# Kernel tuning notes

Hardware: AMD Instinct MI355X
Metric: run time of the kernel (lower is better)

## Reference

```python
import jax, jax.numpy as jnp
import numpy as np

B, S, H = 32, 128, 768
MH, MT = 6, 8            # max holder / target span sizes
M = max(MH, MT)          # max span size -> M conv widths (1..M)
KH, KT = 4, 4            # max n holders / targets per sentence


def _forward(embedding, mask, wh, bh, wt, bt, wi, bi, we, be):
    Bz, Sz, Hz = embedding.shape
    # --- multi-scale span averaging (Conv1d with identity box filters == moving mean) ---
    cs = jnp.concatenate([jnp.zeros((Bz, 1, Hz), embedding.dtype),
                          jnp.cumsum(embedding, axis=1)], axis=1)  # [B,S+1,H]
    reps = [embedding]
    for w in range(2, M + 1):
        mean = (cs[:, w:, :] - cs[:, :-w, :]) / float(w)          # [B,S-w+1,H]
        reps.append(jnp.pad(mean, ((0, 0), (0, w - 1), (0, 0))))  # zero-pad tail like torch.cat
    span = jnp.concatenate(reps, axis=1)                          # [B, M*S, H]; index = S*width_idx + start
    # --- span validity masks (span must fit within sentence length) ---
    lengths = jnp.sum(mask, axis=1)                               # [B]
    pos = jnp.arange(Sz)
    widths = jnp.arange(M)
    base = pos[None, None, :] < (lengths[:, None, None] - widths[None, :, None])  # [B,M,S]
    holder_valid = (base & (widths[None, :, None] < MH)).reshape(Bz, M * Sz)
    target_valid = (base & (widths[None, :, None] < MT)).reshape(Bz, M * Sz)
    # --- span scoring (sigmoid linear), invalid spans forced to -1 ---
    hs = jnp.where(holder_valid, jax.nn.sigmoid(span @ wh + bh), -1.0)  # [B, M*S]
    ts = jnp.where(target_valid, jax.nn.sigmoid(span @ wt + bt), -1.0)
    # --- top-k span selection (== argsort descending, take first K) ---
    vt, it = jax.lax.top_k(ts, KT)
    vh, ih = jax.lax.top_k(hs, KH)
    tval = vt > 0.0                                                # [B,KT]
    hval = vh > 0.0                                                # [B,KH]
    trep = jnp.take_along_axis(span, it[:, :, None], axis=1)      # [B,KT,H]
    hrep = jnp.take_along_axis(span, ih[:, :, None], axis=1)      # [B,KH,H]
    implicit_input = trep * tval[:, :, None].astype(span.dtype)   # zeros where invalid
    pair_valid = (hval[:, :, None] & tval[:, None, :])            # [B,KH,KT]
    pair = jnp.concatenate([jnp.broadcast_to(hrep[:, :, None, :], (Bz, KH, KT, Hz)),
                            jnp.broadcast_to(trep[:, None, :, :], (Bz, KH, KT, Hz))], axis=-1)
    explicit_input = (pair * pair_valid[..., None].astype(span.dtype)).reshape(Bz, KH * KT, 2 * Hz)
    implicit_logits = implicit_input @ wi + bi                    # [B,KT,4]
    explicit_logits = explicit_input @ we + be                    # [B,KH*KT,4]
    return implicit_logits, explicit_logits, hs, ts


def setup_inputs() -> dict:
    key = jax.random.key(0)
    ks = jax.random.split(key, 8)
    embedding = jax.random.normal(ks[0], (B, S, H), jnp.float32)
    mask = jax.random.randint(ks[1], (B, S), 0, 2).astype(jnp.int32)
    wh = jax.random.normal(ks[2], (H,), jnp.float32) * 0.02
    bh = jnp.zeros((), jnp.float32)
    wt = jax.random.normal(ks[3], (H,), jnp.float32) * 0.02
    bt = jnp.zeros((), jnp.float32)
    wi = jax.random.normal(ks[4], (H, 4), jnp.float32) * 0.02
    bi = jnp.zeros((4,), jnp.float32)
    we = jax.random.normal(ks[5], (2 * H, 4), jnp.float32) * 0.02
    be = jnp.zeros((4,), jnp.float32)
    return dict(embedding=embedding, mask=mask, wh=wh, bh=bh, wt=wt, bt=bt,
                wi=wi, bi=bi, we=we, be=be)


def reference(embedding, mask, wh, bh, wt, bt, wi, bi, we, be):
    return _forward(embedding, mask, wh, bh, wt, bt, wi, bi, we, be)
```

## Files before the change

### kernel.cpp

```cpp
#include <hip/hip_runtime.h>

namespace {
constexpr int Bsz = 32;
constexpr int Ssz = 128;
constexpr int Hsz = 768;
constexpr int Msz = 8;
constexpr int MHs = 6;
constexpr int NSPAN = Msz * Ssz;
}

__device__ __forceinline__ bool gtpair(float av, int ai, float bv, int bi) {
    return (av > bv) || (av == bv && ai < bi);
}

struct Top4 { float v[4]; int ix[4]; };

__device__ __forceinline__ void t4_init(Top4& t) {
#pragma unroll
    for (int k = 0; k < 4; ++k) { t.v[k] = -3.f; t.ix[k] = 0x7fffffff; }
}

__device__ __forceinline__ void t4_insert(Top4& t, float cv, int ci) {
    if (!gtpair(cv, ci, t.v[3], t.ix[3])) return;
    if (gtpair(cv, ci, t.v[2], t.ix[2])) {
        t.v[3] = t.v[2]; t.ix[3] = t.ix[2];
        if (gtpair(cv, ci, t.v[1], t.ix[1])) {
            t.v[2] = t.v[1]; t.ix[2] = t.ix[1];
            if (gtpair(cv, ci, t.v[0], t.ix[0])) {
                t.v[1] = t.v[0]; t.ix[1] = t.ix[0];
                t.v[0] = cv; t.ix[0] = ci;
            } else { t.v[1] = cv; t.ix[1] = ci; }
        } else { t.v[2] = cv; t.ix[2] = ci; }
    } else { t.v[3] = cv; t.ix[3] = ci; }
}

__device__ __forceinline__ Top4 t4_merge(const Top4& a, const Top4& b) {
    Top4 r; int pa = 0, pb = 0;
#pragma unroll
    for (int k = 0; k < 4; ++k) {
        float av = a.v[pa]; int ai = a.ix[pa];
        float bv = b.v[pb]; int bi_ = b.ix[pb];
        bool ta = gtpair(av, ai, bv, bi_);
        r.v[k] = ta ? av : bv;
        r.ix[k] = ta ? ai : bi_;
        pa += ta ? 1 : 0; pb += ta ? 0 : 1;
    }
    return r;
}

__device__ __forceinline__ Top4 t4_wave_merge(Top4 t) {
#pragma unroll
    for (int off = 1; off < 64; off <<= 1) {
        Top4 o;
#pragma unroll
        for (int k = 0; k < 4; ++k) {
            o.v[k]  = __shfl_xor(t.v[k], off);
            o.ix[k] = __shfl_xor(t.ix[k], off);
        }
        t = t4_merge(t, o);
    }
    return t;
}

__global__ __launch_bounds__(256) void row_dots_kernel(
    const float* __restrict__ emb, const float* __restrict__ wh,
    const float* __restrict__ wt, float* __restrict__ dh, float* __restrict__ dt)
{
    int row  = blockIdx.x * 4 + (threadIdx.x >> 6);
    int lane = threadIdx.x & 63;
    const float4* r  = (const float4*)(emb + (size_t)row * Hsz);
    const float4* h4 = (const float4*)wh;
    const float4* t4 = (const float4*)wt;
    float ph = 0.f, pt = 0.f;
#pragma unroll
    for (int i = 0; i < 3; ++i) {
        float4 e = r[lane + 64 * i];
        float4 a = h4[lane + 64 * i];
        float4 c = t4[lane + 64 * i];
        ph = fmaf(e.x, a.x, fmaf(e.y, a.y, fmaf(e.z, a.z, fmaf(e.w, a.w, ph))));
        pt = fmaf(e.x, c.x, fmaf(e.y, c.y, fmaf(e.z, c.z, fmaf(e.w, c.w, pt))));
    }
#pragma unroll
    for (int off = 32; off; off >>= 1) {
        ph += __shfl_down(ph, off);
        pt += __shfl_down(pt, off);
    }
    if (lane == 0) { dh[row] = ph; dt[row] = pt; }
}

__global__ __launch_bounds__(256) void per_batch_kernel(
    const float* __restrict__ emb, const int* __restrict__ mask,
    const float* __restrict__ bh_p, const float* __restrict__ bt_p,
    const float* __restrict__ wi, const float* __restrict__ bi,
    const float* __restrict__ we, const float* __restrict__ be,
    const float* __restrict__ dh, const float* __restrict__ dt,
    float* __restrict__ out)
{
    const int b = blockIdx.x;
    const int tid = threadIdx.x;
    const int wavei = tid >> 6, lane = tid & 63;

    __shared__ float dsh[Ssz], dst_[Ssz];
    __shared__ int   len_s;
    __shared__ float swv[2][4][4];
    __shared__ int   swi[2][4][4];
    __shared__ int   sel[8];
    __shared__ int   val[8];
    __shared__ float proj[8][8];

    if (tid < Ssz) {
        dsh[tid]  = dh[b * Ssz + tid];
        dst_[tid] = dt[b * Ssz + tid];
    }
    if (wavei == 0) {
        int m = mask[b * Ssz + lane] + mask[b * Ssz + lane + 64];
#pragma unroll
        for (int off = 32; off; off >>= 1) m += __shfl_down(m, off);
        if (lane == 0) len_s = m;
    }
    __syncthreads();

    const int   len = len_s;
    const float bhv = bh_p[0], btv = bt_p[0];
    float* out_impl = out;
    float* out_expl = out + Bsz * 16;
    float* out_hs   = out_expl + Bsz * 64;
    float* out_ts   = out_hs + Bsz * NSPAN;

    Top4 tt, th;
    t4_init(tt); t4_init(th);
#pragma unroll
    for (int q = 0; q < 4; ++q) {
        int i = tid + 256 * q;
        int widx = i >> 7, st = i & (Ssz - 1), w = widx + 1;
        float h = -1.f, t = -1.f;
        if (st < len - widx) {
            float s_t = 0.f;
            for (int r = 0; r < w; ++r) s_t += dst_[st + r];
            float xt = s_t / (float)w + btv;
            t = 1.f / (1.f + __expf(-xt));
            if (widx < MHs) {
                float s_h = 0.f;
                for (int r = 0; r < w; ++r) s_h += dsh[st + r];
                float xh = s_h / (float)w + bhv;
                h = 1.f / (1.f + __expf(-xh));
            }
        }
        out_hs[b * NSPAN + i] = h;
        out_ts[b * NSPAN + i] = t;
        t4_insert(tt, t, i);
        t4_insert(th, h, i);
    }
    tt = t4_wave_merge(tt);
    th = t4_wave_merge(th);
    if (lane == 0) {
#pragma unroll
        for (int k = 0; k < 4; ++k) {
            swv[0][wavei][k] = tt.v[k]; swi[0][wavei][k] = tt.ix[k];
            swv[1][wavei][k] = th.v[k]; swi[1][wavei][k] = th.ix[k];
        }
    }
    __syncthreads();

    if (tid < 2) {
        Top4 m;
#pragma unroll
        for (int k = 0; k < 4; ++k) { m.v[k] = swv[tid][0][k]; m.ix[k] = swi[tid][0][k]; }
        for (int w2 = 1; w2 < 4; ++w2) {
            Top4 o;
#pragma unroll
            for (int k = 0; k < 4; ++k) { o.v[k] = swv[tid][w2][k]; o.ix[k] = swi[tid][w2][k]; }
            m = t4_merge(m, o);
        }
#pragma unroll
        for (int k = 0; k < 4; ++k) {
            sel[tid * 4 + k] = m.ix[k];
            val[tid * 4 + k] = (m.v[k] > 0.f) ? 1 : 0;
        }
    }
    __syncthreads();

    for (int s2 = 0; s2 < 2; ++s2) {
        int slot = wavei + 4 * s2;
        float acc[8] = {0.f, 0.f, 0.f, 0.f, 0.f, 0.f, 0.f, 0.f};
        if (val[slot]) {
            int idx = sel[slot];
            int w = (idx >> 7) + 1, st = idx & (Ssz - 1);
            const float* base = emb + ((size_t)b * Ssz + st) * Hsz;
#pragma unroll
            for (int ii = 0; ii < Hsz / 64; ++ii) {
                int d = lane + 64 * ii;
                float s = 0.f;
                for (int r = 0; r < w; ++r) s += base[r * Hsz + d];
                float rep = s / (float)w;
                if (s2 == 0) {
                    float4 w4 = ((const float4*)wi)[d];
                    float4 e4 = ((const float4*)we)[Hsz + d];
                    acc[0] = fmaf(rep, w4.x, acc[0]); acc[1] = fmaf(rep, w4.y, acc[1]);
                    acc[2] = fmaf(rep, w4.z, acc[2]); acc[3] = fmaf(rep, w4.w, acc[3]);
                    acc[4] = fmaf(rep, e4.x, acc[4]); acc[5] = fmaf(rep, e4.y, acc[5]);
                    acc[6] = fmaf(rep, e4.z, acc[6]); acc[7] = fmaf(rep, e4.w, acc[7]);
                } else {
                    float4 e4 = ((const float4*)we)[d];
                    acc[0] = fmaf(rep, e4.x, acc[0]); acc[1] = fmaf(rep, e4.y, acc[1]);
                    acc[2] = fmaf(rep, e4.z, acc[2]); acc[3] = fmaf(rep, e4.w, acc[3]);
                }
            }
        }
#pragma unroll
        for (int off = 32; off; off >>= 1)
#pragma unroll
            for (int c = 0; c < 8; ++c) acc[c] += __shfl_down(acc[c], off);
        if (lane == 0)
#pragma unroll
            for (int c = 0; c < 8; ++c) proj[slot][c] = acc[c];
    }
    __syncthreads();

    if (tid < 16) {
        int k = tid >> 2, c = tid & 3;
        out_impl[b * 16 + tid] = bi[c] + (val[k] ? proj[k][c] : 0.f);
    } else if (tid >= 64 && tid < 128) {
        int u = tid - 64;
        int j = u >> 4, k = (u >> 2) & 3, c = u & 3;
        float v = be[c];
        if (val[4 + j] && val[k]) v += proj[4 + j][c] + proj[k][4 + c];
        out_expl[b * 64 + u] = v;
    }
}

extern "C" void kernel_launch(void* const* d_in, const int* in_sizes, int n_in,
                              void* d_out, int out_size, void* d_ws, size_t ws_size,
                              hipStream_t stream) {
    const float* emb  = (const float*)d_in[0];
    const int*   mask = (const int*)d_in[1];
    const float* wh   = (const float*)d_in[2];
    const float* bh   = (const float*)d_in[3];
    const float* wt   = (const float*)d_in[4];
    const float* bt   = (const float*)d_in[5];
    const float* wi   = (const float*)d_in[6];
    const float* bi   = (const float*)d_in[7];
    const float* we   = (const float*)d_in[8];
    const float* be   = (const float*)d_in[9];
    float* out = (float*)d_out;

    float* dh = (float*)d_ws;
    float* dt = dh + Bsz * Ssz;

    row_dots_kernel<<<(Bsz * Ssz) / 4, 256, 0, stream>>>(emb, wh, wt, dh, dt);
    per_batch_kernel<<<Bsz, 256, 0, stream>>>(emb, mask, bh, bt, wi, bi, we, be,
                                              dh, dt, out);
}
```

Before: 104.2 us.

## Use running prefix sums for span scores and vectorize span gather

Span scoring now assigns each thread a single start position and one score type (target or holder), keeping a running sum across widths. This replaces the per-width inner loops over shared memory. Each wave produces one top-4, and the final merge combines pairs of waves. In the projection stage the span embedding gather uses float4 loads and a fully unrolled width loop that masks rows past the span width, so more loads can be in flight. The cost is redundant loads of the last row for short spans and more registers.

```diff
diff --git a/kernel.cpp b/kernel.cpp
--- a/kernel.cpp
+++ b/kernel.cpp
@@ -102,8 +102,8 @@
 
     __shared__ float dsh[Ssz], dst_[Ssz];
     __shared__ int   len_s;
-    __shared__ float swv[2][4][4];
-    __shared__ int   swi[2][4][4];
+    __shared__ float swv[4][4];
+    __shared__ int   swi[4][4];
     __shared__ int   sel[8];
     __shared__ int   val[8];
     __shared__ float proj[8][8];
@@ -127,51 +127,44 @@
     float* out_hs   = out_expl + Bsz * 64;
     float* out_ts   = out_hs + Bsz * NSPAN;
 
-    Top4 tt, th;
-    t4_init(tt); t4_init(th);
-#pragma unroll
-    for (int q = 0; q < 4; ++q) {
-        int i = tid + 256 * q;
-        int widx = i >> 7, st = i & (Ssz - 1), w = widx + 1;
-        float h = -1.f, t = -1.f;
-        if (st < len - widx) {
-            float s_t = 0.f;
-            for (int r = 0; r < w; ++r) s_t += dst_[st + r];
-            float xt = s_t / (float)w + btv;
-            t = 1.f / (1.f + __expf(-xt));
-            if (widx < MHs) {
-                float s_h = 0.f;
-                for (int r = 0; r < w; ++r) s_h += dsh[st + r];
-                float xh = s_h / (float)w + bhv;
-                h = 1.f / (1.f + __expf(-xh));
+    {
+        const int st  = tid & (Ssz - 1);
+        const int grp = tid >> 7;
+        const float* dar = grp ? dsh : dst_;
+        const float  bv  = grp ? bhv : btv;
+        float* outp = grp ? (out_hs + b * NSPAN) : (out_ts + b * NSPAN);
+        Top4 t4l; t4_init(t4l);
+        float run = 0.f;
+#pragma unroll
+        for (int widx = 0; widx < Msz; ++widx) {
+            bool fits = (st < len - widx);
+            if (fits) run += dar[st + widx];
+            bool valid = fits && (grp == 0 || widx < MHs);
+            float sc = -1.f;
+            if (valid) {
+                float x = run * (1.f / (float)(widx + 1)) + bv;
+                sc = 1.f / (1.f + __expf(-x));
             }
-        }
-        out_hs[b * NSPAN + i] = h;
-        out_ts[b * NSPAN + i] = t;
-        t4_insert(tt, t, i);
-        t4_insert(th, h, i);
-    }
-    tt = t4_wave_merge(tt);
-    th = t4_wave_merge(th);
-    if (lane == 0) {
+            int i = (widx << 7) | st;
+            outp[i] = sc;
+            t4_insert(t4l, sc, i);
+        }
+        t4l = t4_wave_merge(t4l);
+        if (lane == 0) {
+#pragma unroll
+            for (int k = 0; k < 4; ++k) { swv[wavei][k] = t4l.v[k]; swi[wavei][k] = t4l.ix[k]; }
+        }
+    }
+    __syncthreads();
+
+    if (tid < 2) {
+        Top4 a, c;
 #pragma unroll
         for (int k = 0; k < 4; ++k) {
-            swv[0][wavei][k] = tt.v[k]; swi[0][wavei][k] = tt.ix[k];
-            swv[1][wavei][k] = th.v[k]; swi[1][wavei][k] = th.ix[k];
-        }
-    }
-    __syncthreads();
-
-    if (tid < 2) {
-        Top4 m;
-#pragma unroll
-        for (int k = 0; k < 4; ++k) { m.v[k] = swv[tid][0][k]; m.ix[k] = swi[tid][0][k]; }
-        for (int w2 = 1; w2 < 4; ++w2) {
-            Top4 o;
-#pragma unroll
-            for (int k = 0; k < 4; ++k) { o.v[k] = swv[tid][w2][k]; o.ix[k] = swi[tid][w2][k]; }
-            m = t4_merge(m, o);
-        }
+            a.v[k] = swv[2 * tid][k];     a.ix[k] = swi[2 * tid][k];
+            c.v[k] = swv[2 * tid + 1][k]; c.ix[k] = swi[2 * tid + 1][k];
+        }
+        Top4 m = t4_merge(a, c);
 #pragma unroll
         for (int k = 0; k < 4; ++k) {
             sel[tid * 4 + k] = m.ix[k];
@@ -186,24 +179,50 @@
         if (val[slot]) {
             int idx = sel[slot];
             int w = (idx >> 7) + 1, st = idx & (Ssz - 1);
-            const float* base = emb + ((size_t)b * Ssz + st) * Hsz;
-#pragma unroll
-            for (int ii = 0; ii < Hsz / 64; ++ii) {
-                int d = lane + 64 * ii;
-                float s = 0.f;
-                for (int r = 0; r < w; ++r) s += base[r * Hsz + d];
-                float rep = s / (float)w;
+            const float4* base = (const float4*)(emb + ((size_t)b * Ssz + st) * Hsz);
+            float inv = 1.f / (float)w;
+            float4 s0 = {0,0,0,0}, s1 = {0,0,0,0}, s2v = {0,0,0,0};
+#pragma unroll
+            for (int r = 0; r < Msz; ++r) {
+                int   rr = (r < w) ? r : (w - 1);
+                float m_ = (r < w) ? inv : 0.f;
+                const float4* rp = base + rr * (Hsz / 4);
+                float4 e0 = rp[lane];
+                float4 e1 = rp[lane + 64];
+                float4 e2 = rp[lane + 128];
+                s0.x = fmaf(e0.x, m_, s0.x); s0.y = fmaf(e0.y, m_, s0.y);
+                s0.z = fmaf(e0.z, m_, s0.z); s0.w = fmaf(e0.w, m_, s0.w);
+                s1.x = fmaf(e1.x, m_, s1.x); s1.y = fmaf(e1.y, m_, s1.y);
+                s1.z = fmaf(e1.z, m_, s1.z); s1.w = fmaf(e1.w, m_, s1.w);
+                s2v.x = fmaf(e2.x, m_, s2v.x); s2v.y = fmaf(e2.y, m_, s2v.y);
+                s2v.z = fmaf(e2.z, m_, s2v.z); s2v.w = fmaf(e2.w, m_, s2v.w);
+            }
+            const float4* wi4 = (const float4*)wi;
+            const float4* we4 = (const float4*)we;
+#pragma unroll
+            for (int ii = 0; ii < 3; ++ii) {
+                float4 rep = (ii == 0) ? s0 : ((ii == 1) ? s1 : s2v);
+                float reps[4] = {rep.x, rep.y, rep.z, rep.w};
+                int j = lane + 64 * ii;
                 if (s2 == 0) {
-                    float4 w4 = ((const float4*)wi)[d];
-                    float4 e4 = ((const float4*)we)[Hsz + d];
-                    acc[0] = fmaf(rep, w4.x, acc[0]); acc[1] = fmaf(rep, w4.y, acc[1]);
-                    acc[2] = fmaf(rep, w4.z, acc[2]); acc[3] = fmaf(rep, w4.w, acc[3]);
-                    acc[4] = fmaf(rep, e4.x, acc[4]); acc[5] = fmaf(rep, e4.y, acc[5]);
-                    acc[6] = fmaf(rep, e4.z, acc[6]); acc[7] = fmaf(rep, e4.w, acc[7]);
+#pragma unroll
+                    for (int t = 0; t < 4; ++t) {
+                        float rt = reps[t];
+                        float4 a = wi4[4 * j + t];
+                        float4 c = we4[Hsz + 4 * j + t];
+                        acc[0] = fmaf(rt, a.x, acc[0]); acc[1] = fmaf(rt, a.y, acc[1]);
+                        acc[2] = fmaf(rt, a.z, acc[2]); acc[3] = fmaf(rt, a.w, acc[3]);
+                        acc[4] = fmaf(rt, c.x, acc[4]); acc[5] = fmaf(rt, c.y, acc[5]);
+                        acc[6] = fmaf(rt, c.z, acc[6]); acc[7] = fmaf(rt, c.w, acc[7]);
+                    }
                 } else {
-                    float4 e4 = ((const float4*)we)[d];
-                    acc[0] = fmaf(rep, e4.x, acc[0]); acc[1] = fmaf(rep, e4.y, acc[1]);
-                    acc[2] = fmaf(rep, e4.z, acc[2]); acc[3] = fmaf(rep, e4.w, acc[3]);
+#pragma unroll
+                    for (int t = 0; t < 4; ++t) {
+                        float rt = reps[t];
+                        float4 c = we4[4 * j + t];
+                        acc[0] = fmaf(rt, c.x, acc[0]); acc[1] = fmaf(rt, c.y, acc[1]);
+                        acc[2] = fmaf(rt, c.z, acc[2]); acc[3] = fmaf(rt, c.w, acc[3]);
+                    }
                 }
             }
         }
```

Result: faster. 97.30 us (-6.6%).
